# Kernel optimization log

Measured on AMD Instinct MI355X. Metric: run time of the kernel, lower is better.

The kernel has to match this reference:

```python
import jax, jax.numpy as jnp
import numpy as np

# ---- constants baked from __init__ (sample_rate=44100, plate_params=None) ----
SR = 44100
K = 1.0 / SR                      # time step
LX = 1.0
FMAX = 10000.0
MAX_OM = FMAX * 2.0 * np.pi
TAU0, TAU1, LOSS_F1 = 6.0, 2.0, 500.0
_OM2 = 2.0 * np.pi * LOSS_F1
_DOMSQ = _OM2 ** 2                # OmDamp1 = 0
ALPHA = 3.0 * np.log(10.0) / _DOMSQ * (_OM2 ** 2 / TAU0)
BETA = 3.0 * np.log(10.0) / _DOMSQ * (1.0 / TAU1 - 1.0 / TAU0)
M_MAX = N_MAX = 80                # 6400 modes
_gm, _gn = np.meshgrid(np.arange(1, M_MAX + 1), np.arange(1, N_MAX + 1), indexing='ij')
M_VEC = jnp.asarray(_gm.reshape(-1), dtype=jnp.float32)
N_VEC = jnp.asarray(_gn.reshape(-1), dtype=jnp.float32)
PI = np.float32(np.pi)


def setup_inputs() -> dict:
    key = jax.random.key(0)
    ks = jax.random.split(key, 6)
    names = ['mu_raw', 'D_over_mu_raw', 'T0_over_mu_raw', 'Ly_raw', 'xo_raw', 'yo_raw']
    inp = {n: jax.random.normal(k, (), dtype=jnp.float32) for n, k in zip(names, ks)}
    inp['num_samples'] = 22050   # duration = 0.5 s at 44100 Hz
    return inp


def reference(mu_raw, D_over_mu_raw, T0_over_mu_raw, Ly_raw, xo_raw, yo_raw, num_samples):
    # physical parameter transforms
    mu = jax.nn.softplus(mu_raw) + 1e-4
    D_over_mu = jax.nn.softplus(D_over_mu_raw) + 1e-4
    T0_over_mu = jax.nn.softplus(T0_over_mu_raw) + 1e-4
    Ly = 1.1 + (4.0 - 1.1) * ((jnp.tanh(Ly_raw) + 1.0) / 2.0)
    xo = 0.49 * LX + (1.0 - 0.49) * LX * ((jnp.tanh(xo_raw) + 1.0) / 2.0)
    yo = 0.51 * Ly + (1.0 - 0.51) * Ly * ((jnp.tanh(yo_raw) + 1.0) / 2.0)

    xi = 0.335 * LX
    yi = 0.467 * Ly

    # modal frequencies / damping, shape [6400]
    g1 = (M_VEC * PI / LX) ** 2 + (N_VEC * PI / Ly) ** 2
    omega_sq = T0_over_mu * g1 + D_over_mu * g1 * g1
    omega = jnp.sqrt(jax.nn.relu(omega_sq))
    temp = 100.0
    valid = jax.nn.sigmoid((MAX_OM - omega) / temp) * jax.nn.sigmoid((omega - 20.0 * 2.0 * PI) / temp)

    in_w = jnp.cos(xi * PI * M_VEC / LX) * jnp.cos(yi * PI * N_VEC / Ly)
    out_w = jnp.cos(xo * PI * M_VEC / LX) * jnp.cos(yo * PI * N_VEC / Ly)
    sigma = ALPHA + BETA * omega ** 2
    ms = 0.25 * mu * LX * Ly
    P = out_w * in_w * (K ** 2) * jnp.exp(-sigma * K) / ms * valid

    # damped sinusoid bank: [6400 modes, num_samples] grids, summed over modes
    n = jnp.arange(num_samples, dtype=jnp.float32)                  # [T]
    coef = P / (jnp.sin(omega * K) + 1e-8)                          # [M]
    env = jnp.exp(-sigma[:, None] * (n[None, :] * K))               # [M, T]
    sine = jnp.sin((n[None, :] + 1.0) * (omega[:, None] * K))       # [M, T]
    disp = jnp.einsum('m,mt,mt->t', coef, env, sine)                # [T]

    # velocity via first difference (velCalc=True)
    prev = jnp.concatenate([jnp.zeros((1,), dtype=disp.dtype), disp[:-1]])
    ir = (disp - prev) / K

    # peak normalization (normalize=True)
    return ir / (jnp.max(jnp.abs(ir)) + 1e-8)
```

## Files before the change

### kernel.cpp

```cpp
#include <hip/hip_runtime.h>
#include <math.h>

#define PI_D      3.14159265358979323846
#define K_D       (1.0 / 44100.0)
#define MAX_OM_D  (10000.0 * 2.0 * PI_D)
#define LN10      2.30258509299404568402
#define ALPHA_D   (3.0 * LN10 / 6.0)
#define OM2_D     (2.0 * PI_D * 500.0)
#define BETA_D    (3.0 * LN10 / (OM2_D * OM2_D) * (1.0 / 2.0 - 1.0 / 6.0))
#define LOG2E_D   1.44269504088896340736
#define INV2PI_D  0.15915494309189533577

#define NMODES  6400
#define TPB     256
#define NS      12
#define TILE    (TPB * NS)
#define NCHUNK  64
#define CHUNK_M (NMODES / NCHUNK)

#if defined(__has_builtin) && __has_builtin(__builtin_amdgcn_sinf)
#define SIN_REV(x) __builtin_amdgcn_sinf(x)
#else
#define SIN_REV(x) __sinf((x) * 6.28318530717958647692f)
#endif
#if defined(__has_builtin) && __has_builtin(__builtin_amdgcn_cosf)
#define COS_REV(x) __builtin_amdgcn_cosf(x)
#else
#define COS_REV(x) __cosf((x) * 6.28318530717958647692f)
#endif
#if defined(__has_builtin) && __has_builtin(__builtin_amdgcn_exp2f)
#define EXP2F(x) __builtin_amdgcn_exp2f(x)
#else
#define EXP2F(x) exp2f(x)
#endif
#if defined(__has_builtin) && __has_builtin(__builtin_amdgcn_fractf)
#define FRACTF(x) __builtin_amdgcn_fractf(x)
#else
#define FRACTF(x) ((x) - floorf(x))
#endif

__device__ inline double softplus_fast(double x) {
    float xf = (float)x;
    float r = (xf > 0.0f) ? xf + log1pf(__expf(-xf)) : log1pf(__expf(xf));
    return (double)r;
}
__device__ inline float cosrev_d(double x) { return COS_REV((float)(x - floor(x))); }
__device__ inline float sinrev_d(double x) { return SIN_REV((float)(x - floor(x))); }
__device__ inline float sigmoid_f(double x) { return 1.0f / (1.0f + __expf((float)(-x))); }

__global__ void mode_params_kernel(const float* __restrict__ mu_raw,
                                   const float* __restrict__ Dmu_raw,
                                   const float* __restrict__ Tmu_raw,
                                   const float* __restrict__ Ly_raw,
                                   const float* __restrict__ xo_raw,
                                   const float* __restrict__ yo_raw,
                                   double* __restrict__ phase64,
                                   float4* __restrict__ pdA,
                                   float4* __restrict__ pdB,
                                   float* __restrict__ disp,
                                   unsigned int* __restrict__ gmax, int T) {
    int i = blockIdx.x * blockDim.x + threadIdx.x;

    for (int k = i; k < T; k += gridDim.x * blockDim.x) disp[k] = 0.0f;
    if (i == 0) *gmax = 0u;

    if (i >= NMODES) return;

    double mu  = softplus_fast((double)mu_raw[0])  + 1e-4;
    double Dmu = softplus_fast((double)Dmu_raw[0]) + 1e-4;
    double Tmu = softplus_fast((double)Tmu_raw[0]) + 1e-4;
    double Ly  = 1.1 + (4.0 - 1.1) * (((double)tanhf(Ly_raw[0]) + 1.0) * 0.5);
    double xo  = 0.49 + 0.51 * (((double)tanhf(xo_raw[0]) + 1.0) * 0.5);
    double yoL = 0.51 + 0.49 * (((double)tanhf(yo_raw[0]) + 1.0) * 0.5);

    int m = i / 80 + 1, n = i % 80 + 1;
    double md = (double)m, nd = (double)n;
    double invLy = 1.0 / Ly;
    double a  = md * PI_D;
    double b  = nd * PI_D * invLy;
    double g1 = a * a + b * b;
    double omsq  = Tmu * g1 + Dmu * g1 * g1;
    double omega = sqrt(omsq > 0.0 ? omsq : 0.0);

    float valid = sigmoid_f((MAX_OM_D - omega) * 0.01) *
                  sigmoid_f((omega - 40.0 * PI_D) * 0.01);
    float in_w  = cosrev_d(0.1675 * md) * cosrev_d(0.2335 * nd);
    float out_w = cosrev_d(0.5 * xo * md) * cosrev_d(0.5 * yoL * nd);

    double sigma = ALPHA_D + BETA_D * omega * omega;
    double ph64  = omega * K_D * INV2PI_D;
    float envK = __expf((float)(-sigma * K_D));
    float P    = out_w * in_w * (float)(K_D * K_D / (0.25 * mu * Ly)) * envK * valid;
    float coef = P / (sinrev_d(ph64) + 1e-8f);
    float dec2 = (float)(-sigma * K_D * LOG2E_D);

    float r256 = EXP2F(dec2 * 256.0f);
    double p256 = ph64 * 256.0;
    float d256 = (float)(p256 - floor(p256));
    float c1 = 2.0f * r256 * COS_REV(d256);
    float c2 = r256 * r256;

    phase64[i] = ph64;
    pdA[i] = make_float4(coef, dec2, c1, c2);
    pdB[i] = make_float4((float)ph64, d256, r256, 0.0f);
}

__global__ __launch_bounds__(TPB) void synth_kernel(const double* __restrict__ phase64,
                                                    const float4* __restrict__ pdA,
                                                    const float4* __restrict__ pdB,
                                                    float* __restrict__ disp, int T) {
    __shared__ float4 sA[CHUNK_M];
    __shared__ float4 sB[CHUNK_M];
    __shared__ int    s_cnt;

    const int m0 = blockIdx.y * CHUNK_M;
    const int t0 = blockIdx.x * TILE;
    const int tid = threadIdx.x;

    if (tid == 0) s_cnt = 0;
    __syncthreads();

    if (tid < CHUNK_M) {
        float4 p = pdA[m0 + tid];
        float cb = p.x * EXP2F(p.y * (float)t0);
        if (cb != 0.0f) {
            float4 q = pdB[m0 + tid];
            double bd = phase64[m0 + tid] * (double)(t0 + 1);
            float base = (float)(bd - floor(bd));
            int idx = atomicAdd(&s_cnt, 1);
            sA[idx] = make_float4(base, cb, p.z, p.w);
            sB[idx] = make_float4(q.x, q.y, q.z, p.y);
        }
    }
    __syncthreads();
    const int n_act = s_cnt;

    float acc[NS];
    #pragma unroll
    for (int i = 0; i < NS; ++i) acc[i] = 0.0f;
    const float tidf = (float)tid;

    for (int j = 0; j < n_act; ++j) {
        float4 a = sA[j];
        float4 b = sB[j];
        float ang0 = fmaf(b.x, tidf, a.x);
        float s0 = SIN_REV(FRACTF(ang0));
        float s1 = SIN_REV(FRACTF(ang0 + b.y));
        float ce = a.y * EXP2F(b.w * tidf);
        float y0 = ce * s0;
        float y1 = ce * b.z * s1;
        acc[0] += y0;
        acc[1] += y1;
        #pragma unroll
        for (int i = 2; i < NS; ++i) {
            float y2 = fmaf(a.z, y1, -(a.w * y0));
            acc[i] += y2;
            y0 = y1; y1 = y2;
        }
    }
    #pragma unroll
    for (int i = 0; i < NS; ++i) {
        int t = t0 + tid + TPB * i;
        if (t < T) atomicAdd(&disp[t], acc[i]);
    }
}

__global__ void diff_max_kernel(const float* __restrict__ disp,
                                float* __restrict__ out,
                                unsigned int* __restrict__ gmax, int T) {
    __shared__ float s_red[TPB / 64];
    int t = blockIdx.x * blockDim.x + threadIdx.x;
    float v = 0.0f;
    if (t < T) {
        float p = (t > 0) ? disp[t - 1] : 0.0f;
        v = (disp[t] - p) * 44100.0f;
        out[t] = v;
    }
    float lmax = fabsf(v);
    for (int o = 32; o > 0; o >>= 1)
        lmax = fmaxf(lmax, __shfl_down(lmax, o, 64));
    if ((threadIdx.x & 63) == 0) s_red[threadIdx.x >> 6] = lmax;
    __syncthreads();
    if (threadIdx.x == 0) {
        float m0 = fmaxf(fmaxf(s_red[0], s_red[1]), fmaxf(s_red[2], s_red[3]));
        atomicMax(gmax, __float_as_uint(m0));
    }
}

__global__ void normalize_kernel(float* __restrict__ out,
                                 const unsigned int* __restrict__ gmax, int T) {
    int t = blockIdx.x * blockDim.x + threadIdx.x;
    if (t >= T) return;
    out[t] = out[t] / (__uint_as_float(*gmax) + 1e-8f);
}

extern "C" void kernel_launch(void* const* d_in, const int* in_sizes, int n_in,
                              void* d_out, int out_size, void* d_ws, size_t ws_size,
                              hipStream_t stream) {
    const float* mu_raw  = (const float*)d_in[0];
    const float* Dmu_raw = (const float*)d_in[1];
    const float* Tmu_raw = (const float*)d_in[2];
    const float* Ly_raw  = (const float*)d_in[3];
    const float* xo_raw  = (const float*)d_in[4];
    const float* yo_raw  = (const float*)d_in[5];
    float* out = (float*)d_out;
    int T = out_size;
    if (T <= 0) return;

    char* ws = (char*)d_ws;
    double* phase64 = (double*)(ws + 0);
    float4* pdA     = (float4*)(ws + 51200);
    float4* pdB     = (float4*)(ws + 153600);
    unsigned int* gmax = (unsigned int*)(ws + 256000);
    float*  disp    = (float*)(ws + 256256);

    int nb = ((T > NMODES ? T : NMODES) + TPB - 1) / TPB;
    mode_params_kernel<<<nb, TPB, 0, stream>>>(
        mu_raw, Dmu_raw, Tmu_raw, Ly_raw, xo_raw, yo_raw,
        phase64, pdA, pdB, disp, gmax, T);

    dim3 grid((T + TILE - 1) / TILE, NCHUNK);
    synth_kernel<<<grid, TPB, 0, stream>>>(phase64, pdA, pdB, disp, T);

    int nb2 = (T + TPB - 1) / TPB;
    diff_max_kernel<<<nb2, TPB, 0, stream>>>(disp, out, gmax, T);
    normalize_kernel<<<nb2, TPB, 0, stream>>>(out, gmax, T);
}
```

Baseline: 93.50 us.

## Fuse all four stages into one cooperative kernel with grid-wide syncs

```diff
diff --git a/kernel.cpp b/kernel.cpp
--- a/kernel.cpp
+++ b/kernel.cpp
@@ -1,5 +1,8 @@
 #include <hip/hip_runtime.h>
+#include <hip/hip_cooperative_groups.h>
 #include <math.h>
+
+namespace cg = cooperative_groups;
 
 #define PI_D      3.14159265358979323846
 #define K_D       (1.0 / 44100.0)
@@ -48,6 +51,159 @@
 __device__ inline float sinrev_d(double x) { return SIN_REV((float)(x - floor(x))); }
 __device__ inline float sigmoid_f(double x) { return 1.0f / (1.0f + __expf((float)(-x))); }
 
+__device__ inline void mode_params_body(int i,
+                                        const float* mu_raw, const float* Dmu_raw,
+                                        const float* Tmu_raw, const float* Ly_raw,
+                                        const float* xo_raw, const float* yo_raw,
+                                        double* phase64, float4* pdA, float4* pdB) {
+    double mu  = softplus_fast((double)mu_raw[0])  + 1e-4;
+    double Dmu = softplus_fast((double)Dmu_raw[0]) + 1e-4;
+    double Tmu = softplus_fast((double)Tmu_raw[0]) + 1e-4;
+    double Ly  = 1.1 + (4.0 - 1.1) * (((double)tanhf(Ly_raw[0]) + 1.0) * 0.5);
+    double xo  = 0.49 + 0.51 * (((double)tanhf(xo_raw[0]) + 1.0) * 0.5);
+    double yoL = 0.51 + 0.49 * (((double)tanhf(yo_raw[0]) + 1.0) * 0.5);
+
+    int m = i / 80 + 1, n = i % 80 + 1;
+    double md = (double)m, nd = (double)n;
+    double invLy = 1.0 / Ly;
+    double a  = md * PI_D;
+    double b  = nd * PI_D * invLy;
+    double g1 = a * a + b * b;
+    double omsq  = Tmu * g1 + Dmu * g1 * g1;
+    double omega = sqrt(omsq > 0.0 ? omsq : 0.0);
+
+    float valid = sigmoid_f((MAX_OM_D - omega) * 0.01) *
+                  sigmoid_f((omega - 40.0 * PI_D) * 0.01);
+    float in_w  = cosrev_d(0.1675 * md) * cosrev_d(0.2335 * nd);
+    float out_w = cosrev_d(0.5 * xo * md) * cosrev_d(0.5 * yoL * nd);
+
+    double sigma = ALPHA_D + BETA_D * omega * omega;
+    double ph64  = omega * K_D * INV2PI_D;
+    float envK = __expf((float)(-sigma * K_D));
+    float P    = out_w * in_w * (float)(K_D * K_D / (0.25 * mu * Ly)) * envK * valid;
+    float coef = P / (sinrev_d(ph64) + 1e-8f);
+    float dec2 = (float)(-sigma * K_D * LOG2E_D);
+
+    float r256 = EXP2F(dec2 * 256.0f);
+    double p256 = ph64 * 256.0;
+    float d256 = (float)(p256 - floor(p256));
+    float c1 = 2.0f * r256 * COS_REV(d256);
+    float c2 = r256 * r256;
+
+    phase64[i] = ph64;
+    pdA[i] = make_float4(coef, dec2, c1, c2);
+    pdB[i] = make_float4((float)ph64, d256, r256, 0.0f);
+}
+
+__global__ __launch_bounds__(TPB) void fused_kernel(const float* __restrict__ mu_raw,
+                                                    const float* __restrict__ Dmu_raw,
+                                                    const float* __restrict__ Tmu_raw,
+                                                    const float* __restrict__ Ly_raw,
+                                                    const float* __restrict__ xo_raw,
+                                                    const float* __restrict__ yo_raw,
+                                                    double* __restrict__ phase64,
+                                                    float4* __restrict__ pdA,
+                                                    float4* __restrict__ pdB,
+                                                    float* __restrict__ disp,
+                                                    float* __restrict__ out,
+                                                    unsigned int* __restrict__ gmax,
+                                                    int T, int ntx) {
+    cg::grid_group grid = cg::this_grid();
+
+    __shared__ float4 sA[CHUNK_M];
+    __shared__ float4 sB[CHUNK_M];
+    __shared__ int    s_cnt;
+    __shared__ float  s_red[TPB / 64];
+
+    const int tid      = threadIdx.x;
+    const int gtid     = blockIdx.x * TPB + tid;
+    const int nthreads = gridDim.x * TPB;
+
+    for (int k = gtid; k < T; k += nthreads) disp[k] = 0.0f;
+    if (gtid == 0) *gmax = 0u;
+    if (gtid < NMODES)
+        mode_params_body(gtid, mu_raw, Dmu_raw, Tmu_raw, Ly_raw, xo_raw, yo_raw,
+                         phase64, pdA, pdB);
+    grid.sync();
+
+    {
+        const int m0 = (blockIdx.x / ntx) * CHUNK_M;
+        const int t0 = (blockIdx.x % ntx) * TILE;
+
+        if (tid == 0) s_cnt = 0;
+        __syncthreads();
+
+        if (tid < CHUNK_M) {
+            float4 p = pdA[m0 + tid];
+            float cb = p.x * EXP2F(p.y * (float)t0);
+            if (cb != 0.0f) {
+                float4 q = pdB[m0 + tid];
+                double bd = phase64[m0 + tid] * (double)(t0 + 1);
+                float base = (float)(bd - floor(bd));
+                int idx = atomicAdd(&s_cnt, 1);
+                sA[idx] = make_float4(base, cb, p.z, p.w);
+                sB[idx] = make_float4(q.x, q.y, q.z, p.y);
+            }
+        }
+        __syncthreads();
+        const int n_act = s_cnt;
+
+        float acc[NS];
+        #pragma unroll
+        for (int i = 0; i < NS; ++i) acc[i] = 0.0f;
+        const float tidf = (float)tid;
+
+        for (int j = 0; j < n_act; ++j) {
+            float4 a = sA[j];
+            float4 b = sB[j];
+            float ang0 = fmaf(b.x, tidf, a.x);
+            float s0 = SIN_REV(FRACTF(ang0));
+            float s1 = SIN_REV(FRACTF(ang0 + b.y));
+            float ce = a.y * EXP2F(b.w * tidf);
+            float y0 = ce * s0;
+            float y1 = ce * b.z * s1;
+            acc[0] += y0;
+            acc[1] += y1;
+            #pragma unroll
+            for (int i = 2; i < NS; ++i) {
+                float y2 = fmaf(a.z, y1, -(a.w * y0));
+                acc[i] += y2;
+                y0 = y1; y1 = y2;
+            }
+        }
+        #pragma unroll
+        for (int i = 0; i < NS; ++i) {
+            int t = t0 + tid + TPB * i;
+            if (t < T) atomicAdd(&disp[t], acc[i]);
+        }
+    }
+    grid.sync();
+
+    {
+        float lmax = 0.0f;
+        for (int t = gtid; t < T; t += nthreads) {
+            float p = (t > 0) ? disp[t - 1] : 0.0f;
+            float v = (disp[t] - p) * 44100.0f;
+            out[t] = v;
+            lmax = fmaxf(lmax, fabsf(v));
+        }
+        for (int o = 32; o > 0; o >>= 1)
+            lmax = fmaxf(lmax, __shfl_down(lmax, o, 64));
+        if ((tid & 63) == 0) s_red[tid >> 6] = lmax;
+        __syncthreads();
+        if (tid == 0) {
+            float m0 = fmaxf(fmaxf(s_red[0], s_red[1]), fmaxf(s_red[2], s_red[3]));
+            atomicMax(gmax, __float_as_uint(m0));
+        }
+    }
+    grid.sync();
+
+    {
+        float mx = __uint_as_float(*gmax) + 1e-8f;
+        for (int t = gtid; t < T; t += nthreads) out[t] = out[t] / mx;
+    }
+}
+
 __global__ void mode_params_kernel(const float* __restrict__ mu_raw,
                                    const float* __restrict__ Dmu_raw,
                                    const float* __restrict__ Tmu_raw,
@@ -60,49 +216,11 @@
                                    float* __restrict__ disp,
                                    unsigned int* __restrict__ gmax, int T) {
     int i = blockIdx.x * blockDim.x + threadIdx.x;
-
     for (int k = i; k < T; k += gridDim.x * blockDim.x) disp[k] = 0.0f;
     if (i == 0) *gmax = 0u;
-
     if (i >= NMODES) return;
-
-    double mu  = softplus_fast((double)mu_raw[0])  + 1e-4;
-    double Dmu = softplus_fast((double)Dmu_raw[0]) + 1e-4;
-    double Tmu = softplus_fast((double)Tmu_raw[0]) + 1e-4;
-    double Ly  = 1.1 + (4.0 - 1.1) * (((double)tanhf(Ly_raw[0]) + 1.0) * 0.5);
-    double xo  = 0.49 + 0.51 * (((double)tanhf(xo_raw[0]) + 1.0) * 0.5);
-    double yoL = 0.51 + 0.49 * (((double)tanhf(yo_raw[0]) + 1.0) * 0.5);
-
-    int m = i / 80 + 1, n = i % 80 + 1;
-    double md = (double)m, nd = (double)n;
-    double invLy = 1.0 / Ly;
-    double a  = md * PI_D;
-    double b  = nd * PI_D * invLy;
-    double g1 = a * a + b * b;
-    double omsq  = Tmu * g1 + Dmu * g1 * g1;
-    double omega = sqrt(omsq > 0.0 ? omsq : 0.0);
-
-    float valid = sigmoid_f((MAX_OM_D - omega) * 0.01) *
-                  sigmoid_f((omega - 40.0 * PI_D) * 0.01);
-    float in_w  = cosrev_d(0.1675 * md) * cosrev_d(0.2335 * nd);
-    float out_w = cosrev_d(0.5 * xo * md) * cosrev_d(0.5 * yoL * nd);
-
-    double sigma = ALPHA_D + BETA_D * omega * omega;
-    double ph64  = omega * K_D * INV2PI_D;
-    float envK = __expf((float)(-sigma * K_D));
-    float P    = out_w * in_w * (float)(K_D * K_D / (0.25 * mu * Ly)) * envK * valid;
-    float coef = P / (sinrev_d(ph64) + 1e-8f);
-    float dec2 = (float)(-sigma * K_D * LOG2E_D);
-
-    float r256 = EXP2F(dec2 * 256.0f);
-    double p256 = ph64 * 256.0;
-    float d256 = (float)(p256 - floor(p256));
-    float c1 = 2.0f * r256 * COS_REV(d256);
-    float c2 = r256 * r256;
-
-    phase64[i] = ph64;
-    pdA[i] = make_float4(coef, dec2, c1, c2);
-    pdB[i] = make_float4((float)ph64, d256, r256, 0.0f);
+    mode_params_body(i, mu_raw, Dmu_raw, Tmu_raw, Ly_raw, xo_raw, yo_raw,
+                     phase64, pdA, pdB);
 }
 
 __global__ __launch_bounds__(TPB) void synth_kernel(const double* __restrict__ phase64,
@@ -214,12 +332,24 @@
     unsigned int* gmax = (unsigned int*)(ws + 256000);
     float*  disp    = (float*)(ws + 256256);
 
+    int ntx = (T + TILE - 1) / TILE;
+    dim3 cgrid(ntx * NCHUNK);
+
+    void* args[] = {(void*)&mu_raw, (void*)&Dmu_raw, (void*)&Tmu_raw,
+                    (void*)&Ly_raw, (void*)&xo_raw, (void*)&yo_raw,
+                    (void*)&phase64, (void*)&pdA, (void*)&pdB,
+                    (void*)&disp, (void*)&out, (void*)&gmax,
+                    (void*)&T, (void*)&ntx};
+    hipError_t err = hipLaunchCooperativeKernel((void*)fused_kernel, cgrid, dim3(TPB),
+                                                args, 0, stream);
+    if (err == hipSuccess) return;
+
     int nb = ((T > NMODES ? T : NMODES) + TPB - 1) / TPB;
     mode_params_kernel<<<nb, TPB, 0, stream>>>(
         mu_raw, Dmu_raw, Tmu_raw, Ly_raw, xo_raw, yo_raw,
         phase64, pdA, pdB, disp, gmax, T);
 
-    dim3 grid((T + TILE - 1) / TILE, NCHUNK);
+    dim3 grid(ntx, NCHUNK);
     synth_kernel<<<grid, TPB, 0, stream>>>(phase64, pdA, pdB, disp, T);
 
     int nb2 = (T + TPB - 1) / TPB;
```

Result: slower. 236.4 us (+152.9%).
